# Optimization experiments

Measured on AMD Instinct MI355X. Metric: run time of the kernel, lower is better.

Reference implementation:

```python
import jax, jax.numpy as jnp
import numpy as np

_SAMPLING_EPS = 1e-5


def setup_inputs() -> dict:
    key = jax.random.key(0)
    ks = jax.random.split(key, 7)
    N, V, H = 256, 128000, 200  # num_seqs, vocab_size, output-history length
    logits = jax.random.normal(ks[0], (N, V), dtype=jnp.float32)
    output_tokens = jax.random.randint(ks[1], (N, H), 0, V, dtype=jnp.int32)
    presence_penalties = jax.random.uniform(ks[2], (N,), jnp.float32, 0.0, 2.0)
    frequency_penalties = jax.random.uniform(ks[3], (N,), jnp.float32, 0.0, 2.0)
    temperatures = jax.random.uniform(ks[4], (N,), jnp.float32, 0.5, 1.5)
    top_ps = jax.random.uniform(ks[5], (N,), jnp.float32, 0.5, 1.0)
    top_ks = jax.random.randint(ks[6], (N,), 1, 1000, dtype=jnp.int32)
    return {
        "logits": logits,
        "presence_penalties": presence_penalties,
        "frequency_penalties": frequency_penalties,
        "temperatures": temperatures,
        "top_ps": top_ps,
        "output_tokens": output_tokens,
        "top_ks": top_ks,
    }


def reference(logits, presence_penalties, frequency_penalties, temperatures,
              top_ps, output_tokens, top_ks):
    N, V = logits.shape

    # ---- _apply_penalties: bincount of previously generated tokens per row ----
    rows = jnp.arange(N)[:, None]  # [N,1] broadcast against [N,H] token ids
    bin_counts = jnp.zeros((N, V), logits.dtype).at[rows, output_tokens].add(1.0)
    # rows are skipped when both penalties are < eps (original builds an index list)
    active = ((presence_penalties >= _SAMPLING_EPS) |
              (frequency_penalties >= _SAMPLING_EPS))[:, None]
    presence_mask = (bin_counts > 0.0).astype(logits.dtype)
    penalty = (frequency_penalties[:, None] * bin_counts
               + presence_penalties[:, None] * presence_mask)
    logits = logits - jnp.where(active, penalty, jnp.zeros((), logits.dtype))

    # ---- temperature scaling + softmax ----
    logits = logits / temperatures[:, None]
    probs = jax.nn.softmax(logits, axis=-1)

    # ---- _apply_top_p_top_k: sort desc, cumsum, mask, unsort ----
    probs_idx = jnp.argsort(-probs, axis=-1)                    # descending order
    probs_sort = jnp.take_along_axis(probs, probs_idx, axis=-1)
    probs_sum = jnp.cumsum(probs_sort, axis=-1)
    top_p_mask = (probs_sum - probs_sort) > top_ps[:, None]     # exclusive cumsum > p
    probs_sort = jnp.where(top_p_mask, 0.0, probs_sort)
    top_k_mask = jnp.arange(V, dtype=top_ks.dtype)[None, :] >= top_ks[:, None]
    probs_sort = jnp.where(top_k_mask, 0.0, probs_sort)
    inv_idx = jnp.argsort(probs_idx, axis=-1)                   # unsort permutation
    filtered_probs = jnp.take_along_axis(probs_sort, inv_idx, axis=-1)
    return filtered_probs
```

## Files before the change

kernel.cpp:

```cpp
#include <hip/hip_runtime.h>
#include <stdint.h>

#define NB 8192
#define BSHIFT 19
#define HS 512
#define HM 511
#define CAP 4096
#define NT 1024

typedef unsigned long long ull;

__device__ __forceinline__ unsigned mono_u32(float x) {
    unsigned b = __float_as_uint(x);
    return (b & 0x80000000u) ? ~b : (b | 0x80000000u);
}
__device__ __forceinline__ float inv_mono(unsigned u) {
    unsigned b = (u & 0x80000000u) ? (u & 0x7fffffffu) : ~u;
    return __uint_as_float(b);
}

__device__ __forceinline__ float compute_x(float l, int cnt,
                                           float pres, float freq, float t) {
    float pen = __fadd_rn(__fmul_rn(freq, (float)cnt), (cnt > 0) ? pres : 0.0f);
    return __fdiv_rn(__fsub_rn(l, pen), t);
}

__device__ __forceinline__ void hash_build(int* hkey, int* hval,
                                           const int* trow, int H, int tid) {
    for (int i = tid; i < HS; i += NT) { hkey[i] = -1; hval[i] = 0; }
    __syncthreads();
    for (int i = tid; i < H; i += NT) {
        int v = trow[i];
        unsigned h = ((unsigned)v * 2654435761u) >> 23;
        while (true) {
            int prev = atomicCAS(&hkey[h], -1, v);
            if (prev == -1 || prev == v) { atomicAdd(&hval[h], 1); break; }
            h = (h + 1) & HM;
        }
    }
    __syncthreads();
}

__device__ __forceinline__ int hash_lookup(const int* hkey, const int* hval, int v) {
    unsigned h = ((unsigned)v * 2654435761u) >> 23;
    while (true) {
        int kk = hkey[h];
        if (kk == v) return hval[h];
        if (kk == -1) return 0;
        h = (h + 1) & HM;
    }
}

__global__ __launch_bounds__(NT) void k_pass1(
    const float* __restrict__ logits, const int* __restrict__ tokens,
    const float* __restrict__ pres_v, const float* __restrict__ freq_v,
    const float* __restrict__ temps, const int* __restrict__ topks,
    int V, int H, float* __restrict__ Sp_o, int* __restrict__ bstar_o)
{
    __shared__ unsigned hc[NB];
    __shared__ int hkey[HS], hval[HS];
    __shared__ int sct[NT], sct2[NT];
    __shared__ float esum_s, corr_s;
    __shared__ int bstar_s;

    int row = blockIdx.x, tid = threadIdx.x;
    for (int b = tid; b < NB; b += NT) hc[b] = 0u;
    if (tid == 0) { esum_s = 0.0f; corr_s = 0.0f; bstar_s = -1; }
    hash_build(hkey, hval, tokens + (size_t)row * H, H, tid);

    float t = temps[row];
    float r = __fdiv_rn(1.0f, t);
    const float4* l4p = (const float4*)(logits + (size_t)row * V);
    int V4 = V >> 2;
    float es = 0.0f;
    int i = tid;
    for (; i + 3 * NT < V4; i += 4 * NT) {
        float4 A = l4p[i], B = l4p[i + NT], C = l4p[i + 2 * NT], D = l4p[i + 3 * NT];
        float4 arr[4] = {A, B, C, D};
#pragma unroll
        for (int q = 0; q < 4; ++q)
#pragma unroll
            for (int j = 0; j < 4; ++j) {
                float x = __fmul_rn((&arr[q].x)[j], r);
                atomicAdd(&hc[mono_u32(x) >> BSHIFT], 1u);
                es += __expf(x);
            }
    }
    for (; i < V4; i += NT) {
        float4 A = l4p[i];
#pragma unroll
        for (int j = 0; j < 4; ++j) {
            float x = __fmul_rn((&A.x)[j], r);
            atomicAdd(&hc[mono_u32(x) >> BSHIFT], 1u);
            es += __expf(x);
        }
    }
    for (int v = (V4 << 2) + tid; v < V; v += NT) {
        float x = __fmul_rn(logits[(size_t)row * V + v], r);
        atomicAdd(&hc[mono_u32(x) >> BSHIFT], 1u);
        es += __expf(x);
    }
    for (int off = 32; off; off >>= 1) es += __shfl_down(es, off);
    if ((tid & 63) == 0) atomicAdd(&esum_s, es);
    __syncthreads();

    float pres = pres_v[row], freq = freq_v[row];
    int active = (pres >= 1e-5f) || (freq >= 1e-5f);
    float corr = 0.0f;
    if (active) {
        for (int s = tid; s < HS; s += NT) {
            int v = hkey[s];
            if (v >= 0) {
                int c = hval[s];
                float l = logits[(size_t)row * V + v];
                float x0 = __fmul_rn(l, r);
                float xp = compute_x(l, c, pres, freq, t);
                unsigned b0 = mono_u32(x0) >> BSHIFT;
                unsigned bp = mono_u32(xp) >> BSHIFT;
                if (b0 != bp) { atomicSub(&hc[b0], 1u); atomicAdd(&hc[bp], 1u); }
                corr += __expf(xp) - __expf(x0);
            }
        }
    }
    for (int off = 32; off; off >>= 1) corr += __shfl_down(corr, off);
    if ((tid & 63) == 0) atomicAdd(&corr_s, corr);
    __syncthreads();

    const int BPT = NB / NT;
    int base = tid * BPT;
    int acc = 0;
#pragma unroll
    for (int q = BPT - 1; q >= 0; --q) { acc += (int)hc[base + q]; hc[base + q] = (unsigned)acc; }
    sct[tid] = acc;
    __syncthreads();
    int* a = sct; int* b2 = sct2;
    for (int s = 1; s < NT; s <<= 1) {
        int v = a[tid] + ((tid + s < NT) ? a[tid + s] : 0);
        __syncthreads();
        b2[tid] = v;
        __syncthreads();
        int* tmp = a; a = b2; b2 = tmp;
    }
    int above = (tid < NT - 1) ? a[tid + 1] : 0;
    int k = topks[row];
    int best = -1;
#pragma unroll
    for (int q = BPT - 1; q >= 0; --q)
        if ((int)hc[base + q] + above >= k) { best = base + q; break; }
    if (best >= 0) atomicMax(&bstar_s, best);
    __syncthreads();
    if (tid == 0) {
        Sp_o[row] = esum_s + corr_s;
        bstar_o[row] = bstar_s;
    }
}

__global__ __launch_bounds__(NT) void k_pass2(
    const float* __restrict__ logits, const int* __restrict__ tokens,
    const float* __restrict__ pres_v, const float* __restrict__ freq_v,
    const float* __restrict__ temps, const float* __restrict__ topp_v,
    const int* __restrict__ topk_v, int V, int H,
    const float* __restrict__ Sp_i, const int* __restrict__ bstar_i,
    float* __restrict__ out)
{
    __shared__ ull skey[CAP];
    __shared__ float se[CAP];
    __shared__ float bs1[NT], bs2[NT];
    __shared__ int hkey[HS], hval[HS];
    __shared__ int lcnt_s;

    int row = blockIdx.x, tid = threadIdx.x;
    if (tid == 0) lcnt_s = 0;
    hash_build(hkey, hval, tokens + (size_t)row * H, H, tid);

    float t = temps[row];
    float r = __fdiv_rn(1.0f, t);
    int bst = bstar_i[row] - 2;
    if (bst < 0) bst = 0;
    const float4* l4p = (const float4*)(logits + (size_t)row * V);
    float4* o4p = (float4*)(out + (size_t)row * V);
    int V4 = V >> 2;
    const float4 z4 = make_float4(0.f, 0.f, 0.f, 0.f);

    int i = tid;
    for (; i + 3 * NT < V4; i += 4 * NT) {
        float4 A = l4p[i], B = l4p[i + NT], C = l4p[i + 2 * NT], D = l4p[i + 3 * NT];
        o4p[i] = z4; o4p[i + NT] = z4; o4p[i + 2 * NT] = z4; o4p[i + 3 * NT] = z4;
        float4 arr[4] = {A, B, C, D};
#pragma unroll
        for (int q = 0; q < 4; ++q) {
            int vb = (i + q * NT) << 2;
#pragma unroll
            for (int j = 0; j < 4; ++j) {
                float l = (&arr[q].x)[j];
                unsigned ua = mono_u32(__fmul_rn(l, r));
                if ((int)(ua >> BSHIFT) >= bst) {
                    unsigned ue = mono_u32(__fdiv_rn(l, t));
                    int pos = atomicAdd(&lcnt_s, 1);
                    if (pos < CAP)
                        skey[pos] = ((ull)ue << 32) | (unsigned)~(unsigned)(vb + j);
                }
            }
        }
    }
    for (; i < V4; i += NT) {
        float4 A = l4p[i];
        o4p[i] = z4;
#pragma unroll
        for (int j = 0; j < 4; ++j) {
            float l = (&A.x)[j];
            unsigned ua = mono_u32(__fmul_rn(l, r));
            if ((int)(ua >> BSHIFT) >= bst) {
                unsigned ue = mono_u32(__fdiv_rn(l, t));
                int pos = atomicAdd(&lcnt_s, 1);
                if (pos < CAP)
                    skey[pos] = ((ull)ue << 32) | (unsigned)~(unsigned)((i << 2) + j);
            }
        }
    }
    for (int v = (V4 << 2) + tid; v < V; v += NT) {
        float l = logits[(size_t)row * V + v];
        out[(size_t)row * V + v] = 0.0f;
        unsigned ua = mono_u32(__fmul_rn(l, r));
        if ((int)(ua >> BSHIFT) >= bst) {
            unsigned ue = mono_u32(__fdiv_rn(l, t));
            int pos = atomicAdd(&lcnt_s, 1);
            if (pos < CAP)
                skey[pos] = ((ull)ue << 32) | (unsigned)~(unsigned)v;
        }
    }
    __syncthreads();
    int count = lcnt_s; if (count > CAP) count = CAP;

    float pres = pres_v[row], freq = freq_v[row];
    int active = (pres >= 1e-5f) || (freq >= 1e-5f);
    if (active) {
        for (int j = tid; j < count; j += NT) {
            unsigned idx = ~(unsigned)(skey[j] & 0xffffffffull);
            int c = hash_lookup(hkey, hval, (int)idx);
            if (c > 0) {
                float l = logits[(size_t)row * V + idx];
                float xp = compute_x(l, c, pres, freq, t);
                skey[j] = ((ull)mono_u32(xp) << 32) | (unsigned)~idx;
            }
        }
    }
    int m = 1; while (m < count) m <<= 1;
    for (int j = count + tid; j < m; j += NT) skey[j] = 0ull;
    __syncthreads();

    for (int kk = 2; kk <= m; kk <<= 1) {
        for (int jj = kk >> 1; jj > 0; jj >>= 1) {
            for (int i2 = tid; i2 < m; i2 += NT) {
                int ixj = i2 ^ jj;
                if (ixj > i2) {
                    ull A = skey[i2], B = skey[ixj];
                    bool up = ((i2 & kk) != 0);
                    if ((A > B) == up) { skey[i2] = B; skey[ixj] = A; }
                }
            }
            __syncthreads();
        }
    }

    for (int j = tid; j < CAP; j += NT)
        se[j] = (j < count) ? __expf(inv_mono((unsigned)(skey[j] >> 32))) : 0.0f;
    __syncthreads();

    int j0 = tid << 2;
    float e0 = se[j0], e1 = se[j0 + 1], e2 = se[j0 + 2], e3 = se[j0 + 3];
    float c0 = e0, c1 = c0 + e1, c2 = c1 + e2, c3 = c2 + e3;
    bs1[tid] = c3;
    __syncthreads();
    float* a = bs1; float* b2 = bs2;
    for (int s = 1; s < NT; s <<= 1) {
        float v = a[tid] + ((tid >= s) ? a[tid - s] : 0.0f);
        __syncthreads();
        b2[tid] = v;
        __syncthreads();
        float* tmp = a; a = b2; b2 = tmp;
    }
    float pre = (tid > 0) ? a[tid - 1] : 0.0f;

    float Sp = Sp_i[row];
    float pS = topp_v[row] * Sp;
    int k = topk_v[row];
    float inc[4] = {pre + c0, pre + c1, pre + c2, pre + c3};
    float ee[4] = {e0, e1, e2, e3};
#pragma unroll
    for (int q = 0; q < 4; ++q) {
        int j = j0 + q;
        if (j < count) {
            float e = ee[q];
            float excl = __fsub_rn(inc[q], e);
            if ((j < k) && (excl <= pS)) {
                unsigned idx = ~(unsigned)(skey[j] & 0xffffffffull);
                out[(size_t)row * V + idx] = __fdiv_rn(e, Sp);
            }
        }
    }
}

extern "C" void kernel_launch(void* const* d_in, const int* in_sizes, int n_in,
                              void* d_out, int out_size, void* d_ws, size_t ws_size,
                              hipStream_t stream) {
    const float* logits = (const float*)d_in[0];
    const float* pres   = (const float*)d_in[1];
    const float* freq   = (const float*)d_in[2];
    const float* temps  = (const float*)d_in[3];
    const float* topps  = (const float*)d_in[4];
    const int*   tokens = (const int*)d_in[5];
    const int*   topks  = (const int*)d_in[6];
    int N = in_sizes[1];
    int V = in_sizes[0] / N;
    int H = in_sizes[5] / N;
    float* out = (float*)d_out;

    char* ws = (char*)d_ws;
    float* Sp    = (float*)ws;
    int*   bstar = (int*)(ws + 4 * (size_t)N);

    k_pass1<<<N, NT, 0, stream>>>(logits, tokens, pres, freq, temps, topks,
                                  V, H, Sp, bstar);
    k_pass2<<<N, NT, 0, stream>>>(logits, tokens, pres, freq, temps, topps, topks,
                                  V, H, Sp, bstar, out);
}
```

Measured before the change: 327.1 us.

## Fuse two-pass top-k/top-p kernel into one and prefilter candidates with fine histogram

```diff
diff --git a/kernel.cpp b/kernel.cpp
--- a/kernel.cpp
+++ b/kernel.cpp
@@ -6,6 +6,8 @@
 #define HS 512
 #define HM 511
 #define CAP 4096
+#define PCAP 2048
+#define NRB 2048
 #define NT 1024
 
 typedef unsigned long long ull;
@@ -25,10 +27,37 @@
     return __fdiv_rn(__fsub_rn(l, pen), t);
 }
 
-__device__ __forceinline__ void hash_build(int* hkey, int* hval,
-                                           const int* trow, int H, int tid) {
+__global__ __launch_bounds__(NT) void k_fused(
+    const float* __restrict__ logits, const int* __restrict__ tokens,
+    const float* __restrict__ pres_v, const float* __restrict__ freq_v,
+    const float* __restrict__ temps, const float* __restrict__ topp_v,
+    const int* __restrict__ topk_v, int V, int H, float* __restrict__ out)
+{
+    __shared__ __align__(16) char smem[(32 + 16 + 8 + 4) * 1024];
+    unsigned* hc = (unsigned*)smem;
+    ull* skey = (ull*)smem;
+    char* regB = smem + 32 * 1024;
+    float* se = (float*)regB;
+    int* sct = (int*)regB;
+    int* sct2 = (int*)(regB + 4 * 1024);
+    ull* tmpc = (ull*)regB;
+    char* regC = smem + 48 * 1024;
+    float* bs1 = (float*)regC;
+    float* bs2 = (float*)(regC + 4 * 1024);
+    unsigned* rh = (unsigned*)regC;
+    char* regD = smem + 56 * 1024;
+    int* hkey = (int*)regD;
+    int* hval = (int*)(regD + 2 * 1024);
+    __shared__ float esum_s, corr_s;
+    __shared__ int bstar_s, lcnt_s, rb_s, pcnt_s;
+
+    int row = blockIdx.x, tid = threadIdx.x;
+    for (int b = tid; b < NB; b += NT) hc[b] = 0u;
+    if (tid == 0) { esum_s = 0.f; corr_s = 0.f; bstar_s = -1; lcnt_s = 0; rb_s = 0; pcnt_s = 0; }
+
     for (int i = tid; i < HS; i += NT) { hkey[i] = -1; hval[i] = 0; }
     __syncthreads();
+    const int* trow = tokens + (size_t)row * H;
     for (int i = tid; i < H; i += NT) {
         int v = trow[i];
         unsigned h = ((unsigned)v * 2654435761u) >> 23;
@@ -39,46 +68,21 @@
         }
     }
     __syncthreads();
-}
-
-__device__ __forceinline__ int hash_lookup(const int* hkey, const int* hval, int v) {
-    unsigned h = ((unsigned)v * 2654435761u) >> 23;
-    while (true) {
-        int kk = hkey[h];
-        if (kk == v) return hval[h];
-        if (kk == -1) return 0;
-        h = (h + 1) & HM;
-    }
-}
-
-__global__ __launch_bounds__(NT) void k_pass1(
-    const float* __restrict__ logits, const int* __restrict__ tokens,
-    const float* __restrict__ pres_v, const float* __restrict__ freq_v,
-    const float* __restrict__ temps, const int* __restrict__ topks,
-    int V, int H, float* __restrict__ Sp_o, int* __restrict__ bstar_o)
-{
-    __shared__ unsigned hc[NB];
-    __shared__ int hkey[HS], hval[HS];
-    __shared__ int sct[NT], sct2[NT];
-    __shared__ float esum_s, corr_s;
-    __shared__ int bstar_s;
-
-    int row = blockIdx.x, tid = threadIdx.x;
-    for (int b = tid; b < NB; b += NT) hc[b] = 0u;
-    if (tid == 0) { esum_s = 0.0f; corr_s = 0.0f; bstar_s = -1; }
-    hash_build(hkey, hval, tokens + (size_t)row * H, H, tid);
 
     float t = temps[row];
     float r = __fdiv_rn(1.0f, t);
-    const float4* l4p = (const float4*)(logits + (size_t)row * V);
+    const float* lrow = logits + (size_t)row * V;
+    const float4* l4p = (const float4*)lrow;
     int V4 = V >> 2;
+
     float es = 0.0f;
     int i = tid;
-    for (; i + 3 * NT < V4; i += 4 * NT) {
-        float4 A = l4p[i], B = l4p[i + NT], C = l4p[i + 2 * NT], D = l4p[i + 3 * NT];
-        float4 arr[4] = {A, B, C, D};
-#pragma unroll
-        for (int q = 0; q < 4; ++q)
+    for (; i + 7 * NT < V4; i += 8 * NT) {
+        float4 arr[8];
+#pragma unroll
+        for (int q = 0; q < 8; ++q) arr[q] = l4p[i + q * NT];
+#pragma unroll
+        for (int q = 0; q < 8; ++q)
 #pragma unroll
             for (int j = 0; j < 4; ++j) {
                 float x = __fmul_rn((&arr[q].x)[j], r);
@@ -96,7 +100,7 @@
         }
     }
     for (int v = (V4 << 2) + tid; v < V; v += NT) {
-        float x = __fmul_rn(logits[(size_t)row * V + v], r);
+        float x = __fmul_rn(lrow[v], r);
         atomicAdd(&hc[mono_u32(x) >> BSHIFT], 1u);
         es += __expf(x);
     }
@@ -112,7 +116,7 @@
             int v = hkey[s];
             if (v >= 0) {
                 int c = hval[s];
-                float l = logits[(size_t)row * V + v];
+                float l = lrow[v];
                 float x0 = __fmul_rn(l, r);
                 float xp = compute_x(l, c, pres, freq, t);
                 unsigned b0 = mono_u32(x0) >> BSHIFT;
@@ -133,62 +137,40 @@
     for (int q = BPT - 1; q >= 0; --q) { acc += (int)hc[base + q]; hc[base + q] = (unsigned)acc; }
     sct[tid] = acc;
     __syncthreads();
-    int* a = sct; int* b2 = sct2;
-    for (int s = 1; s < NT; s <<= 1) {
-        int v = a[tid] + ((tid + s < NT) ? a[tid + s] : 0);
-        __syncthreads();
-        b2[tid] = v;
-        __syncthreads();
-        int* tmp = a; a = b2; b2 = tmp;
-    }
-    int above = (tid < NT - 1) ? a[tid + 1] : 0;
-    int k = topks[row];
-    int best = -1;
-#pragma unroll
-    for (int q = BPT - 1; q >= 0; --q)
-        if ((int)hc[base + q] + above >= k) { best = base + q; break; }
-    if (best >= 0) atomicMax(&bstar_s, best);
-    __syncthreads();
-    if (tid == 0) {
-        Sp_o[row] = esum_s + corr_s;
-        bstar_o[row] = bstar_s;
-    }
-}
-
-__global__ __launch_bounds__(NT) void k_pass2(
-    const float* __restrict__ logits, const int* __restrict__ tokens,
-    const float* __restrict__ pres_v, const float* __restrict__ freq_v,
-    const float* __restrict__ temps, const float* __restrict__ topp_v,
-    const int* __restrict__ topk_v, int V, int H,
-    const float* __restrict__ Sp_i, const int* __restrict__ bstar_i,
-    float* __restrict__ out)
-{
-    __shared__ ull skey[CAP];
-    __shared__ float se[CAP];
-    __shared__ float bs1[NT], bs2[NT];
-    __shared__ int hkey[HS], hval[HS];
-    __shared__ int lcnt_s;
-
-    int row = blockIdx.x, tid = threadIdx.x;
-    if (tid == 0) lcnt_s = 0;
-    hash_build(hkey, hval, tokens + (size_t)row * H, H, tid);
-
-    float t = temps[row];
-    float r = __fdiv_rn(1.0f, t);
-    int bst = bstar_i[row] - 2;
+    {
+        int* a = sct; int* b2 = sct2;
+        for (int s = 1; s < NT; s <<= 1) {
+            int v = a[tid] + ((tid + s < NT) ? a[tid + s] : 0);
+            __syncthreads();
+            b2[tid] = v;
+            __syncthreads();
+            int* tmp = a; a = b2; b2 = tmp;
+        }
+        int above = (tid < NT - 1) ? a[tid + 1] : 0;
+        int k = topk_v[row];
+        int best = -1;
+#pragma unroll
+        for (int q = BPT - 1; q >= 0; --q)
+            if ((int)hc[base + q] + above >= k) { best = base + q; break; }
+        if (best >= 0) atomicMax(&bstar_s, best);
+    }
+    __syncthreads();
+    int bst = bstar_s - 2;
     if (bst < 0) bst = 0;
-    const float4* l4p = (const float4*)(logits + (size_t)row * V);
+    float Sp = esum_s + corr_s;
+    __syncthreads();
+
     float4* o4p = (float4*)(out + (size_t)row * V);
-    int V4 = V >> 2;
     const float4 z4 = make_float4(0.f, 0.f, 0.f, 0.f);
-
-    int i = tid;
-    for (; i + 3 * NT < V4; i += 4 * NT) {
-        float4 A = l4p[i], B = l4p[i + NT], C = l4p[i + 2 * NT], D = l4p[i + 3 * NT];
-        o4p[i] = z4; o4p[i + NT] = z4; o4p[i + 2 * NT] = z4; o4p[i + 3 * NT] = z4;
-        float4 arr[4] = {A, B, C, D};
-#pragma unroll
-        for (int q = 0; q < 4; ++q) {
+    i = tid;
+    for (; i + 7 * NT < V4; i += 8 * NT) {
+        float4 arr[8];
+#pragma unroll
+        for (int q = 0; q < 8; ++q) arr[q] = l4p[i + q * NT];
+#pragma unroll
+        for (int q = 0; q < 8; ++q) o4p[i + q * NT] = z4;
+#pragma unroll
+        for (int q = 0; q < 8; ++q) {
             int vb = (i + q * NT) << 2;
 #pragma unroll
             for (int j = 0; j < 4; ++j) {
@@ -219,7 +201,7 @@
         }
     }
     for (int v = (V4 << 2) + tid; v < V; v += NT) {
-        float l = logits[(size_t)row * V + v];
+        float l = lrow[v];
         out[(size_t)row * V + v] = 0.0f;
         unsigned ua = mono_u32(__fmul_rn(l, r));
         if ((int)(ua >> BSHIFT) >= bst) {
@@ -231,24 +213,80 @@
     }
     __syncthreads();
     int count = lcnt_s; if (count > CAP) count = CAP;
-
-    float pres = pres_v[row], freq = freq_v[row];
-    int active = (pres >= 1e-5f) || (freq >= 1e-5f);
+    int k = topk_v[row];
+
     if (active) {
         for (int j = tid; j < count; j += NT) {
             unsigned idx = ~(unsigned)(skey[j] & 0xffffffffull);
-            int c = hash_lookup(hkey, hval, (int)idx);
+            unsigned h = (idx * 2654435761u) >> 23;
+            int c = 0;
+            while (true) {
+                int kk = hkey[h];
+                if (kk == (int)idx) { c = hval[h]; break; }
+                if (kk == -1) break;
+                h = (h + 1) & HM;
+            }
             if (c > 0) {
-                float l = logits[(size_t)row * V + idx];
-                float xp = compute_x(l, c, pres, freq, t);
+                float xp = compute_x(lrow[idx], c, pres, freq, t);
                 skey[j] = ((ull)mono_u32(xp) << 32) | (unsigned)~idx;
             }
         }
     }
+    __syncthreads();
+    for (int g = tid; g < NRB; g += NT) rh[g] = 0u;
+    __syncthreads();
+    int gmin = bst << 6;
+    for (int j = tid; j < count; j += NT) {
+        unsigned u = (unsigned)(skey[j] >> 32);
+        int rel = (int)(u >> 13) - gmin;
+        rel = rel < 0 ? 0 : (rel > NRB - 1 ? NRB - 1 : rel);
+        atomicAdd(&rh[rel], 1u);
+    }
+    __syncthreads();
+    {
+        int b2i = tid * 2;
+        int a2 = (int)rh[b2i + 1];
+        rh[b2i + 1] = (unsigned)a2;
+        a2 += (int)rh[b2i];
+        rh[b2i] = (unsigned)a2;
+        sct[tid] = a2;
+        __syncthreads();
+        int* a = sct; int* b2 = sct2;
+        for (int s = 1; s < NT; s <<= 1) {
+            int v = a[tid] + ((tid + s < NT) ? a[tid + s] : 0);
+            __syncthreads();
+            b2[tid] = v;
+            __syncthreads();
+            int* tmp = a; a = b2; b2 = tmp;
+        }
+        int above = (tid < NT - 1) ? a[tid + 1] : 0;
+        int best = -1;
+        if ((int)rh[b2i + 1] + above >= k) best = b2i + 1;
+        else if ((int)rh[b2i] + above >= k) best = b2i;
+        if (best >= 0) atomicMax(&rb_s, best);
+    }
+    __syncthreads();
+    int rb = rb_s;
+    for (int j = tid; j < count; j += NT) {
+        unsigned u = (unsigned)(skey[j] >> 32);
+        int rel = (int)(u >> 13) - gmin;
+        rel = rel < 0 ? 0 : (rel > NRB - 1 ? NRB - 1 : rel);
+        if (rel >= rb) {
+            int pos = atomicAdd(&pcnt_s, 1);
+            if (pos < PCAP) tmpc[pos] = skey[j];
+        }
+    }
+    __syncthreads();
+    int count2 = pcnt_s;
+    if (count2 <= PCAP) {
+        for (int j = tid; j < count2; j += NT) skey[j] = tmpc[j];
+        count = count2;
+    }
+    __syncthreads();
+
     int m = 1; while (m < count) m <<= 1;
     for (int j = count + tid; j < m; j += NT) skey[j] = 0ull;
     __syncthreads();
-
     for (int kk = 2; kk <= m; kk <<= 1) {
         for (int jj = kk >> 1; jj > 0; jj >>= 1) {
             for (int i2 = tid; i2 < m; i2 += NT) {
@@ -266,7 +304,6 @@
     for (int j = tid; j < CAP; j += NT)
         se[j] = (j < count) ? __expf(inv_mono((unsigned)(skey[j] >> 32))) : 0.0f;
     __syncthreads();
-
     int j0 = tid << 2;
     float e0 = se[j0], e1 = se[j0 + 1], e2 = se[j0 + 2], e3 = se[j0 + 3];
     float c0 = e0, c1 = c0 + e1, c2 = c1 + e2, c3 = c2 + e3;
@@ -282,9 +319,7 @@
     }
     float pre = (tid > 0) ? a[tid - 1] : 0.0f;
 
-    float Sp = Sp_i[row];
     float pS = topp_v[row] * Sp;
-    int k = topk_v[row];
     float inc[4] = {pre + c0, pre + c1, pre + c2, pre + c3};
     float ee[4] = {e0, e1, e2, e3};
 #pragma unroll
@@ -316,12 +351,6 @@
     int H = in_sizes[5] / N;
     float* out = (float*)d_out;
 
-    char* ws = (char*)d_ws;
-    float* Sp    = (float*)ws;
-    int*   bstar = (int*)(ws + 4 * (size_t)N);
-
-    k_pass1<<<N, NT, 0, stream>>>(logits, tokens, pres, freq, temps, topks,
-                                  V, H, Sp, bstar);
-    k_pass2<<<N, NT, 0, stream>>>(logits, tokens, pres, freq, temps, topps, topks,
-                                  V, H, Sp, bstar, out);
-}
+    k_fused<<<N, NT, 0, stream>>>(logits, tokens, pres, freq, temps, topps,
+                                  topks, V, H, out);
+}
```

After: 295.8 us. 9.6% less time.
